# Kernel optimization log

Hardware: AMD Instinct MI355X
Metric: run time of the kernel (lower is better)

Reference implementation:

```python
import jax, jax.numpy as jnp
import numpy as np

WS = (7, 7, 7)
N = WS[0] * WS[1] * WS[2]          # 343 tokens per window
B, D, L, H = 128, 512, 6, 8
DH = D // H                        # 64
DFF = 4 * D
EPS = 1e-5


def _relative_position_index_3d(ws):
    d = np.arange(ws[0]); h = np.arange(ws[1]); w = np.arange(ws[2])
    coords = np.stack(np.meshgrid(d, h, w, indexing='ij'))      # [3, D, H, W]
    cf = coords.reshape(3, -1)                                   # [3, n]
    rel = cf[:, :, None] - cf[:, None, :]                        # [3, n, n]
    rel = rel.transpose(1, 2, 0).copy()                          # [n, n, 3]
    rel[:, :, 0] += ws[0] - 1
    rel[:, :, 1] += ws[1] - 1
    rel[:, :, 2] += ws[2] - 1
    rel[:, :, 0] *= (2 * ws[1] - 1) * (2 * ws[2] - 1)
    rel[:, :, 1] *= 2 * ws[2] - 1
    return rel.sum(-1).astype(np.int32)                          # [n, n]


def setup_inputs() -> dict:
    key = jax.random.key(0)
    ks = jax.random.split(key, 16)
    s = lambda d: 1.0 / np.sqrt(d)
    inp = {
        'x':    jax.random.normal(ks[0], (B, N, D), jnp.float32),
        'Wq':   jax.random.normal(ks[1], (L, D, D), jnp.float32) * s(D),
        'Wk':   jax.random.normal(ks[2], (L, D, D), jnp.float32) * s(D),
        'Wv':   jax.random.normal(ks[3], (L, D, D), jnp.float32) * s(D),
        'Wo':   jax.random.normal(ks[4], (L, D, D), jnp.float32) * s(D),
        'W1ff': jax.random.normal(ks[5], (L, D, DFF), jnp.float32) * s(D),
        'b1ff': jnp.zeros((L, DFF), jnp.float32),
        'W2ff': jax.random.normal(ks[6], (L, DFF, D), jnp.float32) * s(DFF),
        'b2ff': jnp.zeros((L, D), jnp.float32),
        'ln1_g': jnp.ones((L, D), jnp.float32),
        'ln1_b': jnp.zeros((L, D), jnp.float32),
        'ln2_g': jnp.ones((L, D), jnp.float32),
        'ln2_b': jnp.zeros((L, D), jnp.float32),
        'lnf_g': jnp.ones((D,), jnp.float32),
        'lnf_b': jnp.zeros((D,), jnp.float32),
        'rel_table': jax.random.normal(ks[7], ((2 * WS[0] - 1) * (2 * WS[1] - 1) * (2 * WS[2] - 1), H), jnp.float32) * 0.02,
        'cpb_w1': jax.random.normal(ks[8], (H, 512), jnp.float32) * s(H),
        'cpb_b1': jax.random.normal(ks[9], (512,), jnp.float32) * 0.02,
        'cpb_w2': jax.random.normal(ks[10], (512, H), jnp.float32) * s(512),
        'rel_index': jnp.asarray(_relative_position_index_3d(WS)),
    }
    return inp


def _layer_norm(x, g, b):
    mu = jnp.mean(x, -1, keepdims=True)
    xc = x - mu
    var = jnp.mean(xc * xc, -1, keepdims=True)
    return xc * jax.lax.rsqrt(var + EPS) * g + b


def _rel_pos_bias(rel_table, cpb_w1, cpb_b1, cpb_w2, rel_index):
    # cpb_mlp: Linear(H->512) + ReLU + Linear(512->H, no bias)
    t = jax.nn.relu(rel_table @ cpb_w1 + cpb_b1) @ cpb_w2        # [T, H]
    bias = t[rel_index.reshape(-1)].reshape(N, N, H)             # gather -> [n, n, H]
    return jnp.transpose(bias, (2, 0, 1))                        # [H, n, n]


def reference(x, Wq, Wk, Wv, Wo, W1ff, b1ff, W2ff, b2ff,
              ln1_g, ln1_b, ln2_g, ln2_b, lnf_g, lnf_b,
              rel_table, cpb_w1, cpb_b1, cpb_w2, rel_index):
    bias = _rel_pos_bias(rel_table, cpb_w1, cpb_b1, cpb_w2, rel_index)  # [H, n, n] shared across layers
    scale = DH ** -0.5
    for l in range(L):
        # --- attention block (pre-norm) ---
        h = _layer_norm(x, ln1_g[l], ln1_b[l])
        q = (h @ Wq[l]).reshape(B, N, H, DH)
        k = (h @ Wk[l]).reshape(B, N, H, DH)
        v = (h @ Wv[l]).reshape(B, N, H, DH)
        scores = jnp.einsum('bihd,bjhd->bhij', q, k) * scale + bias[None]
        attn = jax.nn.softmax(scores, axis=-1)
        o = jnp.einsum('bhij,bjhd->bihd', attn, v).reshape(B, N, D)
        x = x + o @ Wo[l]
        # --- feed-forward block (pre-norm) ---
        h = _layer_norm(x, ln2_g[l], ln2_b[l])
        x = x + jax.nn.gelu(h @ W1ff[l] + b1ff[l]) @ W2ff[l] + b2ff[l]
    return _layer_norm(x, lnf_g, lnf_b)
```

## Files before the change

### kernel.cpp

```cpp
#include <hip/hip_runtime.h>

typedef __attribute__((ext_vector_type(8))) short short8;
typedef __attribute__((ext_vector_type(4))) float fx4;
typedef __attribute__((ext_vector_type(4))) int ix4;

#define MFMA16(a, b, c) __builtin_amdgcn_mfma_f32_16x16x32_bf16((a), (b), (c), 0, 0, 0)

__device__ __forceinline__ short f2bf(float f) {
  unsigned u = __float_as_uint(f);
  u += 0x7fffu + ((u >> 16) & 1u);
  return (short)(u >> 16);
}
__device__ __forceinline__ float bf2f(short v) {
  return __uint_as_float(((unsigned)(unsigned short)v) << 16);
}
__device__ __forceinline__ void glds16(const short* g, short* l) {
  __builtin_amdgcn_global_load_lds((const __attribute__((address_space(1))) void*)g,
                                   (__attribute__((address_space(3))) void*)l, 16, 0, 0);
}
__device__ __forceinline__ unsigned lds_off(const void* p) {
  return (unsigned)(uintptr_t)(const __attribute__((address_space(3))) void*)p;
}
__device__ __forceinline__ ix4 ds_read128(unsigned addr) {
  ix4 r;
  asm volatile("ds_read_b128 %0, %1" : "=v"(r) : "v"(addr));
  return r;
}
#define LGKM(N)                                             \
  asm volatile("s_waitcnt lgkmcnt(" #N ")" ::: "memory");   \
  __builtin_amdgcn_sched_barrier(0)

__global__ __launch_bounds__(256)
void transpose_cvt(const float* __restrict__ W, short* __restrict__ Wt, int K, int N) {
  __shared__ float tile[64][65];
  const int kb = blockIdx.x * 64, nb = blockIdx.y * 64;
  const int t = threadIdx.x;
  const int tr = t >> 6, tc = t & 63;
#pragma unroll 4
  for (int i = 0; i < 16; i++) {
    int r = i * 4 + tr;
    tile[r][tc] = W[(size_t)(kb + r) * N + nb + tc];
  }
  __syncthreads();
#pragma unroll 4
  for (int i = 0; i < 16; i++) {
    int r = i * 4 + tr;
    Wt[(size_t)(nb + r) * K + kb + tc] = f2bf(tile[tc][r]);
  }
}

__global__ __launch_bounds__(256)
void cpb_kernel(const float* __restrict__ rt, const float* __restrict__ w1,
                const float* __restrict__ b1, const float* __restrict__ w2,
                float* __restrict__ tt) {
  const int id = blockIdx.x * 256 + threadIdx.x;
  if (id >= 2197 * 8) return;
  const int row = id >> 3, hh = id & 7;
  float r[8];
#pragma unroll
  for (int i = 0; i < 8; i++) r[i] = rt[row * 8 + i];
  float acc = 0.0f;
  for (int c = 0; c < 512; c++) {
    float s = b1[c];
#pragma unroll
    for (int i = 0; i < 8; i++) s += r[i] * w1[i * 512 + c];
    s = fmaxf(s, 0.0f);
    acc += s * w2[c * 8 + hh];
  }
  tt[id] = acc;
}

__global__ __launch_bounds__(256)
void build_biasfrag(const float* __restrict__ tt, const int* __restrict__ ridx,
                    short* __restrict__ biasb) {
  const int id = blockIdx.x * 256 + threadIdx.x;
  if (id >= 8 * 22 * 11 * 512) return;
  const int e = id & 7;
  const int lane = (id >> 3) & 63;
  const int rest = id >> 9;
  const int jp = rest % 11;
  const int rest2 = rest / 11;
  const int qt = rest2 % 22;
  const int h = rest2 / 22;
  const int q = qt * 16 + ((lane >> 4) << 2) + (e & 3);
  const int tok = (jp * 2 + (e >> 2)) * 16 + (lane & 15);
  float val = -1e30f;
  if (q < 343 && tok < 343) val = tt[ridx[q * 343 + tok] * 8 + h];
  biasb[id] = f2bf(val);
}

template <bool BF16OUT>
__global__ __launch_bounds__(256)
void ln_kernel(const float* x, const float* __restrict__ g,
               const float* __restrict__ bb, void* out) {
  const int row = blockIdx.x * 4 + (threadIdx.x >> 6);
  const int lane = threadIdx.x & 63;
  const float* xr = x + (size_t)row * 512 + lane * 8;
  fx4 va = *(const fx4*)xr;
  fx4 vb = *(const fx4*)(xr + 4);
  float s = va[0] + va[1] + va[2] + va[3] + vb[0] + vb[1] + vb[2] + vb[3];
#pragma unroll
  for (int d = 1; d < 64; d <<= 1) s += __shfl_xor(s, d);
  const float mu = s * (1.0f / 512.0f);
  float v[8];
#pragma unroll
  for (int i = 0; i < 4; i++) { v[i] = va[i] - mu; v[4 + i] = vb[i] - mu; }
  float s2 = 0.0f;
#pragma unroll
  for (int i = 0; i < 8; i++) s2 += v[i] * v[i];
#pragma unroll
  for (int d = 1; d < 64; d <<= 1) s2 += __shfl_xor(s2, d);
  const float rs = rsqrtf(s2 * (1.0f / 512.0f) + 1e-5f);
  fx4 ga = *(const fx4*)(g + lane * 8);
  fx4 gb = *(const fx4*)(g + lane * 8 + 4);
  fx4 ba = *(const fx4*)(bb + lane * 8);
  fx4 b2 = *(const fx4*)(bb + lane * 8 + 4);
  float o[8];
#pragma unroll
  for (int i = 0; i < 4; i++) {
    o[i] = v[i] * rs * ga[i] + ba[i];
    o[4 + i] = v[4 + i] * rs * gb[i] + b2[i];
  }
  if (BF16OUT) {
    short8 ov;
#pragma unroll
    for (int i = 0; i < 8; i++) ov[i] = f2bf(o[i]);
    *(short8*)((short*)out + (size_t)row * 512 + lane * 8) = ov;
  } else {
    float* op = (float*)out + (size_t)row * 512 + lane * 8;
    fx4 o1, o2;
#pragma unroll
    for (int i = 0; i < 4; i++) { o1[i] = o[i]; o2[i] = o[4 + i]; }
    *(fx4*)op = o1;
    *(fx4*)(op + 4) = o2;
  }
}

template <int EPI>
__global__ __launch_bounds__(256, 3)
void gemm_s(const short* __restrict__ A, const short* __restrict__ Bt,
            int N, int K, int nbn, int scaleN,
            const float* __restrict__ bias, const float* xres, void* out) {
  __shared__ short Al[3][4096];
  __shared__ short Bl[3][4096];
  const int nwg = gridDim.x;
  const int orig = blockIdx.x;
  const int qq = nwg >> 3, rr = nwg & 7, xc = orig & 7, o8 = orig >> 3;
  const int wgid = (xc < rr ? xc * (qq + 1) : rr * (qq + 1) + (xc - rr) * qq) + o8;
  const int m0 = (wgid / nbn) * 128, n0 = (wgid % nbn) * 128;
  const int t = threadIdx.x, lane = t & 63, wv = t >> 6;
  const int lr = lane & 15, lg = lane >> 4;
  const int scol = ((lane & 3) * 8) ^ ((lane & 32) ? 16 : 0);
  const int srow = lane >> 2;
  const short* ag0 = A + (size_t)(m0 + wv * 32 + srow) * K + scol;
  const short* ag1 = A + (size_t)(m0 + wv * 32 + 16 + srow) * K + scol;
  const short* bg0 = Bt + (size_t)(n0 + wv * 32 + srow) * K + scol;
  const short* bg1 = Bt + (size_t)(n0 + wv * 32 + 16 + srow) * K + scol;
  const int cswz = (lg * 8) ^ ((lr & 8) ? 16 : 0);
  const unsigned abase = lds_off(&Al[0][0]);
  const unsigned bbase = lds_off(&Bl[0][0]);
  unsigned aoffB[4], boffB[4];
#pragma unroll
  for (int i = 0; i < 4; i++) {
    aoffB[i] = (((wv >> 1) * 4 + i) * 512 + lr * 32 + cswz) * 2u;
    boffB[i] = (((wv & 1) * 4 + i) * 512 + lr * 32 + cswz) * 2u;
  }
  fx4 acc[4][4] = {};
#define STAGE(KT, BUF)                              \
  do {                                              \
    const int off_ = (KT) * 32;                     \
    short* la_ = &Al[BUF][wv * 1024];               \
    short* lb_ = &Bl[BUF][wv * 1024];               \
    glds16(ag0 + off_, la_);                        \
    glds16(ag1 + off_, la_ + 512);                  \
    glds16(bg0 + off_, lb_);                        \
    glds16(bg1 + off_, lb_ + 512);                  \
  } while (0)
  const int nkt = K >> 5;
  STAGE(0, 0);
  STAGE(1, 1);
  int rb = 0;
  for (int kt = 0; kt < nkt; kt++) {
    if (kt + 1 < nkt)
      asm volatile("s_waitcnt vmcnt(4)" ::: "memory");
    else
      asm volatile("s_waitcnt vmcnt(0)" ::: "memory");
    __builtin_amdgcn_s_barrier();
    if (kt + 2 < nkt) {
      int sb = rb + 2;
      if (sb >= 3) sb -= 3;
      STAGE(kt + 2, sb);
    }
    const unsigned ab = abase + (unsigned)rb * 8192u;
    const unsigned bb_ = bbase + (unsigned)rb * 8192u;
    ix4 a0 = ds_read128(ab + aoffB[0]);
    ix4 b0 = ds_read128(bb_ + boffB[0]);
    ix4 b1 = ds_read128(bb_ + boffB[1]);
    ix4 b2 = ds_read128(bb_ + boffB[2]);
    ix4 b3 = ds_read128(bb_ + boffB[3]);
    ix4 a1 = ds_read128(ab + aoffB[1]);
    ix4 a2 = ds_read128(ab + aoffB[2]);
    ix4 a3 = ds_read128(ab + aoffB[3]);
    const short8 B0 = __builtin_bit_cast(short8, b0);
    const short8 B1 = __builtin_bit_cast(short8, b1);
    const short8 B2 = __builtin_bit_cast(short8, b2);
    const short8 B3 = __builtin_bit_cast(short8, b3);
    LGKM(3);
    {
      const short8 Af = __builtin_bit_cast(short8, a0);
      acc[0][0] = MFMA16(Af, B0, acc[0][0]);
      acc[0][1] = MFMA16(Af, B1, acc[0][1]);
      acc[0][2] = MFMA16(Af, B2, acc[0][2]);
      acc[0][3] = MFMA16(Af, B3, acc[0][3]);
    }
    LGKM(2);
    {
      const short8 Af = __builtin_bit_cast(short8, a1);
      acc[1][0] = MFMA16(Af, B0, acc[1][0]);
      acc[1][1] = MFMA16(Af, B1, acc[1][1]);
      acc[1][2] = MFMA16(Af, B2, acc[1][2]);
      acc[1][3] = MFMA16(Af, B3, acc[1][3]);
    }
    LGKM(1);
    {
      const short8 Af = __builtin_bit_cast(short8, a2);
      acc[2][0] = MFMA16(Af, B0, acc[2][0]);
      acc[2][1] = MFMA16(Af, B1, acc[2][1]);
      acc[2][2] = MFMA16(Af, B2, acc[2][2]);
      acc[2][3] = MFMA16(Af, B3, acc[2][3]);
    }
    LGKM(0);
    {
      const short8 Af = __builtin_bit_cast(short8, a3);
      acc[3][0] = MFMA16(Af, B0, acc[3][0]);
      acc[3][1] = MFMA16(Af, B1, acc[3][1]);
      acc[3][2] = MFMA16(Af, B2, acc[3][2]);
      acc[3][3] = MFMA16(Af, B3, acc[3][3]);
    }
    rb = (rb + 1 < 3) ? rb + 1 : 0;
  }
#undef STAGE
#pragma unroll
  for (int mi = 0; mi < 4; mi++) {
#pragma unroll
    for (int ni = 0; ni < 4; ni++) {
#pragma unroll
      for (int r = 0; r < 4; r++) {
        const int row = m0 + (wv >> 1) * 64 + mi * 16 + lg * 4 + r;
        const int col = n0 + (wv & 1) * 64 + ni * 16 + lr;
        const float vacc = acc[mi][ni][r];
        const size_t idx = (size_t)row * N + col;
        if (EPI == 0) {
          const float sc = (col < scaleN) ? 0.125f : 1.0f;
          ((short*)out)[idx] = f2bf(vacc * sc);
        } else if (EPI == 1) {
          ((float*)out)[idx] = xres[idx] + vacc;
        } else if (EPI == 2) {
          const float v = vacc + bias[col];
          const float tt = v * v;
          const float u2 = v * fmaf(tt, -0.0713548165f, -1.5957691216f);
          const float g = v * __builtin_amdgcn_rcpf(1.0f + __expf(u2));
          ((short*)out)[idx] = f2bf(g);
        } else {
          ((float*)out)[idx] = xres[idx] + vacc + bias[col];
        }
      }
    }
  }
}

__global__ __launch_bounds__(512, 1)
void attn_kernel(const short* __restrict__ qkv, const short* __restrict__ biasb,
                 short* __restrict__ obuf) {
  __shared__ short Kl[352][72];
  __shared__ short Vt[64][360];
  __shared__ short Pl[8][16][96];
  const int b = blockIdx.x >> 3, h = blockIdx.x & 7;
  const int t = threadIdx.x, lane = t & 63, wv = t >> 6;
  const int lr = lane & 15, lg = lane >> 4;
  const size_t base = (size_t)b * 343 * 1536 + h * 64;
  const short* qg = qkv + base;
  const short* kg = qkv + base + 512;
  const short* vg = qkv + base + 1024;
  for (int c = t; c < 352 * 8; c += 512) {
    const int tok = c >> 3, d8 = (c & 7) * 8;
    const int ts = tok < 343 ? tok : 342;
    short8 kvv = *(const short8*)(kg + (size_t)ts * 1536 + d8);
    short8 vvv = *(const short8*)(vg + (size_t)ts * 1536 + d8);
    *(short8*)&Kl[tok][d8] = kvv;
#pragma unroll
    for (int j = 0; j < 8; j++) Vt[d8 + j][tok] = vvv[j];
  }
  __syncthreads();
  for (int qt = wv; qt < 22; qt += 8) {
    const int q0 = qt * 16;
    const int qr = q0 + lr;
    const int qs = qr < 343 ? qr : 342;
    short8 qf0 = *(const short8*)(qg + (size_t)qs * 1536 + lg * 8);
    short8 qf1 = *(const short8*)(qg + (size_t)qs * 1536 + 32 + lg * 8);
    fx4 s[22];
#pragma unroll
    for (int j = 0; j < 22; j++) {
      short8 kf0 = *(const short8*)&Kl[j * 16 + lr][lg * 8];
      short8 kf1 = *(const short8*)&Kl[j * 16 + lr][32 + lg * 8];
      fx4 z = {0.0f, 0.0f, 0.0f, 0.0f};
      z = MFMA16(qf0, kf0, z);
      z = MFMA16(qf1, kf1, z);
      s[j] = z;
    }
    const short* bp = biasb + (size_t)((h * 22 + qt) * 11) * 512 + lane * 8;
#pragma unroll
    for (int jp = 0; jp < 11; jp++) {
      short8 bb = *(const short8*)(bp + jp * 512);
#pragma unroll
      for (int r = 0; r < 4; r++) {
        s[2 * jp][r] += bf2f(bb[r]);
        s[2 * jp + 1][r] += bf2f(bb[4 + r]);
      }
    }
    float mx[4] = {-1e30f, -1e30f, -1e30f, -1e30f};
#pragma unroll
    for (int j = 0; j < 22; j++)
#pragma unroll
      for (int r = 0; r < 4; r++) mx[r] = fmaxf(mx[r], s[j][r]);
#pragma unroll
    for (int r = 0; r < 4; r++) {
      float m = mx[r];
      m = fmaxf(m, __shfl_xor(m, 1));
      m = fmaxf(m, __shfl_xor(m, 2));
      m = fmaxf(m, __shfl_xor(m, 4));
      m = fmaxf(m, __shfl_xor(m, 8));
      mx[r] = m;
    }
    float sm[4] = {0.0f, 0.0f, 0.0f, 0.0f};
#pragma unroll
    for (int j = 0; j < 22; j++)
#pragma unroll
      for (int r = 0; r < 4; r++) {
        const float p = __expf(s[j][r] - mx[r]);
        s[j][r] = p;
        sm[r] += p;
      }
#pragma unroll
    for (int r = 0; r < 4; r++) {
      float ss = sm[r];
      ss += __shfl_xor(ss, 1);
      ss += __shfl_xor(ss, 2);
      ss += __shfl_xor(ss, 4);
      ss += __shfl_xor(ss, 8);
      sm[r] = 1.0f / ss;
    }
    fx4 oacc[4] = {};
#pragma unroll
    for (int c = 0; c < 4; c++) {
      const int nj = (c < 3) ? 6 : 4;
#pragma unroll
      for (int j = 0; j < 6; j++) {
        if (j < nj) {
#pragma unroll
          for (int r = 0; r < 4; r++)
            Pl[wv][lg * 4 + r][j * 16 + lr] = f2bf(s[c * 6 + j][r] * sm[r]);
        }
      }
      const int nk = (c < 3) ? 3 : 2;
#pragma unroll
      for (int ks = 0; ks < 3; ks++) {
        if (ks < nk) {
          short8 pb = *(const short8*)&Pl[wv][lr][ks * 32 + lg * 8];
#pragma unroll
          for (int mi = 0; mi < 4; mi++) {
            short8 vva = *(const short8*)&Vt[mi * 16 + lr][c * 96 + ks * 32 + lg * 8];
            oacc[mi] = MFMA16(vva, pb, oacc[mi]);
          }
        }
      }
    }
    if (qr < 343) {
#pragma unroll
      for (int mi = 0; mi < 4; mi++)
#pragma unroll
        for (int r = 0; r < 4; r++) {
          const int dh = mi * 16 + lg * 4 + r;
          obuf[(size_t)(b * 343 + qr) * 512 + h * 64 + dh] = f2bf(oacc[mi][r]);
        }
    }
  }
}

extern "C" void kernel_launch(void* const* d_in, const int* in_sizes, int n_in,
                              void* d_out, int out_size, void* d_ws, size_t ws_size,
                              hipStream_t stream) {
  const float* x_in = (const float*)d_in[0];
  const float* Wq = (const float*)d_in[1];
  const float* Wk = (const float*)d_in[2];
  const float* Wv = (const float*)d_in[3];
  const float* Wo = (const float*)d_in[4];
  const float* W1 = (const float*)d_in[5];
  const float* b1 = (const float*)d_in[6];
  const float* W2 = (const float*)d_in[7];
  const float* b2 = (const float*)d_in[8];
  const float* ln1g = (const float*)d_in[9];
  const float* ln1b = (const float*)d_in[10];
  const float* ln2g = (const float*)d_in[11];
  const float* ln2b = (const float*)d_in[12];
  const float* lnfg = (const float*)d_in[13];
  const float* lnfb = (const float*)d_in[14];
  const float* rtab = (const float*)d_in[15];
  const float* cw1 = (const float*)d_in[16];
  const float* cb1 = (const float*)d_in[17];
  const float* cw2 = (const float*)d_in[18];
  const int* ridx = (const int*)d_in[19];
  float* xout = (float*)d_out;

  char* p = (char*)d_ws;
  short* wt = (short*)p;      p += 37748736;
  short* hbuf = (short*)p;    p += 44957696;
  char* big = p;              p += 179830784;
  short* biasb = (short*)p;   p += 1982464;
  float* tt = (float*)p;      p += 70304;
  short* qkvbuf = (short*)big;
  short* obuf = (short*)(big + 134873088);
  short* mid = (short*)big;

  cpb_kernel<<<(2197 * 8 + 255) / 256, 256, 0, stream>>>(rtab, cw1, cb1, cw2, tt);
  build_biasfrag<<<(8 * 22 * 11 * 512 + 255) / 256, 256, 0, stream>>>(tt, ridx, biasb);

  for (int l = 0; l < 6; l++) {
    const size_t wl = (size_t)l * 3145728;
    transpose_cvt<<<dim3(8, 8), 256, 0, stream>>>(Wq + (size_t)l * 262144, wt + wl, 512, 512);
    transpose_cvt<<<dim3(8, 8), 256, 0, stream>>>(Wk + (size_t)l * 262144, wt + wl + 262144, 512, 512);
    transpose_cvt<<<dim3(8, 8), 256, 0, stream>>>(Wv + (size_t)l * 262144, wt + wl + 524288, 512, 512);
    transpose_cvt<<<dim3(8, 8), 256, 0, stream>>>(Wo + (size_t)l * 262144, wt + wl + 786432, 512, 512);
    transpose_cvt<<<dim3(8, 32), 256, 0, stream>>>(W1 + (size_t)l * 1048576, wt + wl + 1048576, 512, 2048);
    transpose_cvt<<<dim3(32, 8), 256, 0, stream>>>(W2 + (size_t)l * 1048576, wt + wl + 2097152, 2048, 512);
  }

  for (int l = 0; l < 6; l++) {
    const size_t wl = (size_t)l * 3145728;
    const float* xsrc = (l == 0) ? x_in : xout;
    ln_kernel<true><<<10976, 256, 0, stream>>>(xsrc, ln1g + l * 512, ln1b + l * 512, hbuf);
    gemm_s<0><<<343 * 12, 256, 0, stream>>>(hbuf, wt + wl, 1536, 512, 12, 512, nullptr, nullptr, qkvbuf);
    attn_kernel<<<1024, 512, 0, stream>>>(qkvbuf, biasb, obuf);
    gemm_s<1><<<343 * 4, 256, 0, stream>>>(obuf, wt + wl + 786432, 512, 512, 4, 0, nullptr, xsrc, xout);
    ln_kernel<true><<<10976, 256, 0, stream>>>(xout, ln2g + l * 512, ln2b + l * 512, hbuf);
    gemm_s<2><<<343 * 16, 256, 0, stream>>>(hbuf, wt + wl + 1048576, 2048, 512, 16, 0, b1 + l * 2048, nullptr, mid);
    gemm_s<3><<<343 * 4, 256, 0, stream>>>(mid, wt + wl + 2097152, 512, 2048, 4, 0, b2 + l * 512, xout, xout);
  }
  ln_kernel<false><<<10976, 256, 0, stream>>>(xout, lnfg, lnfb, xout);
}
```

Measured before the change: 4.077 ms.

## Fuse residual add and layer norm into full-row output projection GEMMs

Adds a gemm_ln kernel in which each workgroup computes a 128x512 full-width output tile, so the residual add, bias and the following LayerNorm (ln2, next layer's ln1, or the final norm) can be applied in the epilogue through a cross-wave LDS reduction. This removes the separate ln_kernel launches and their extra read and write of the fp32 activations. The cost is a grid of only 343 workgroups of 512 threads with large per-thread accumulator state, which lowers parallelism and occupancy compared with the previous 1372-block GEMMs. Variance is computed as E[x^2]-mu^2, which is less numerically robust than a two-pass computation.

```diff
diff --git a/kernel.cpp b/kernel.cpp
--- a/kernel.cpp
+++ b/kernel.cpp
@@ -269,6 +269,199 @@
   }
 }
 
+template <int MODE>
+__global__ __launch_bounds__(512, 2)
+void gemm_ln(const short* __restrict__ A, const short* __restrict__ Bt, int K,
+             const float* __restrict__ bias, const float* xres,
+             const float* __restrict__ lng, const float* __restrict__ lnb,
+             float* xout, short* hbuf) {
+  __shared__ short lds3[3][20480];
+  const int nwg = gridDim.x;
+  const int orig = blockIdx.x;
+  const int qq = nwg >> 3, rr2 = nwg & 7, xcd = orig & 7, o8 = orig >> 3;
+  const int wgid = (xcd < rr2 ? xcd * (qq + 1) : rr2 * (qq + 1) + (xcd - rr2) * qq) + o8;
+  const int m0 = wgid * 128;
+  const int t = threadIdx.x, lane = t & 63, wv = t >> 6;
+  const int wave_m = wv >> 2, wave_n = wv & 3;
+  const int lr = lane & 15, lg = lane >> 4;
+  const int scol = ((lane & 3) * 8) ^ ((lane & 32) ? 16 : 0);
+  const int srow = lane >> 2;
+  const short* gsrc[5];
+#pragma unroll
+  for (int j = 0; j < 5; j++) {
+    const int c = wv * 5 + j;
+    gsrc[j] = (c < 8) ? A + (size_t)(m0 + c * 16 + srow) * K + scol
+                      : Bt + (size_t)((c - 8) * 16 + srow) * K + scol;
+  }
+  const int cswz = (lg * 8) ^ ((lr & 8) ? 16 : 0);
+  const unsigned base0 = lds_off(&lds3[0][0]);
+  unsigned aoff[4], boff[8];
+#pragma unroll
+  for (int i = 0; i < 4; i++)
+    aoff[i] = (unsigned)((wave_m * 4 + i) * 512 + lr * 32 + cswz) * 2u;
+#pragma unroll
+  for (int i = 0; i < 8; i++)
+    boff[i] = (unsigned)(4096 + (wave_n * 8 + i) * 512 + lr * 32 + cswz) * 2u;
+  fx4 acc[4][8];
+#pragma unroll
+  for (int mi = 0; mi < 4; mi++)
+#pragma unroll
+    for (int ni = 0; ni < 8; ni++) acc[mi][ni] = fx4{0.f, 0.f, 0.f, 0.f};
+#define STAGE(KT, BUF)                                    \
+  do {                                                    \
+    const size_t koff = (size_t)(KT) * 32;                \
+    short* ld = &lds3[BUF][wv * 2560];                    \
+    _Pragma("unroll") for (int j_ = 0; j_ < 5; j_++)      \
+        glds16(gsrc[j_] + koff, ld + j_ * 512);           \
+  } while (0)
+  const int nkt = K >> 5;
+  STAGE(0, 0);
+  STAGE(1, 1);
+  int rb = 0;
+  for (int kt = 0; kt < nkt; kt++) {
+    if (kt + 1 < nkt)
+      asm volatile("s_waitcnt vmcnt(5)" ::: "memory");
+    else
+      asm volatile("s_waitcnt vmcnt(0)" ::: "memory");
+    __builtin_amdgcn_s_barrier();
+    if (kt + 2 < nkt) {
+      int sb = rb + 2;
+      if (sb >= 3) sb -= 3;
+      STAGE(kt + 2, sb);
+    }
+    const unsigned bufb = base0 + (unsigned)rb * 40960u;
+    ix4 a0 = ds_read128(bufb + aoff[0]);
+    ix4 b0 = ds_read128(bufb + boff[0]);
+    ix4 b1 = ds_read128(bufb + boff[1]);
+    ix4 b2 = ds_read128(bufb + boff[2]);
+    ix4 b3 = ds_read128(bufb + boff[3]);
+    ix4 b4 = ds_read128(bufb + boff[4]);
+    ix4 b5 = ds_read128(bufb + boff[5]);
+    ix4 b6 = ds_read128(bufb + boff[6]);
+    ix4 b7 = ds_read128(bufb + boff[7]);
+    ix4 a1 = ds_read128(bufb + aoff[1]);
+    ix4 a2 = ds_read128(bufb + aoff[2]);
+    ix4 a3 = ds_read128(bufb + aoff[3]);
+    const short8 B0 = __builtin_bit_cast(short8, b0);
+    const short8 B1 = __builtin_bit_cast(short8, b1);
+    const short8 B2 = __builtin_bit_cast(short8, b2);
+    const short8 B3 = __builtin_bit_cast(short8, b3);
+    const short8 B4 = __builtin_bit_cast(short8, b4);
+    const short8 B5 = __builtin_bit_cast(short8, b5);
+    const short8 B6 = __builtin_bit_cast(short8, b6);
+    const short8 B7 = __builtin_bit_cast(short8, b7);
+#define ROW(mi, av)                                                  \
+  {                                                                  \
+    const short8 Af = __builtin_bit_cast(short8, av);                \
+    acc[mi][0] = MFMA16(Af, B0, acc[mi][0]);                         \
+    acc[mi][1] = MFMA16(Af, B1, acc[mi][1]);                         \
+    acc[mi][2] = MFMA16(Af, B2, acc[mi][2]);                         \
+    acc[mi][3] = MFMA16(Af, B3, acc[mi][3]);                         \
+    acc[mi][4] = MFMA16(Af, B4, acc[mi][4]);                         \
+    acc[mi][5] = MFMA16(Af, B5, acc[mi][5]);                         \
+    acc[mi][6] = MFMA16(Af, B6, acc[mi][6]);                         \
+    acc[mi][7] = MFMA16(Af, B7, acc[mi][7]);                         \
+  }
+    LGKM(3);
+    ROW(0, a0);
+    LGKM(2);
+    ROW(1, a1);
+    LGKM(1);
+    ROW(2, a2);
+    LGKM(0);
+    ROW(3, a3);
+#undef ROW
+    rb = (rb + 1 < 3) ? rb + 1 : 0;
+  }
+#undef STAGE
+  __syncthreads();
+  float gc[8], bc[8], bcol[8];
+#pragma unroll
+  for (int ni = 0; ni < 8; ni++) {
+    const int col = wave_n * 128 + ni * 16 + lr;
+    gc[ni] = lng[col];
+    bc[ni] = lnb[col];
+    bcol[ni] = (MODE != 0) ? bias[col] : 0.0f;
+  }
+  float s_[4][4], q_[4][4];
+#pragma unroll
+  for (int mi = 0; mi < 4; mi++)
+#pragma unroll
+    for (int rr = 0; rr < 4; rr++) { s_[mi][rr] = 0.f; q_[mi][rr] = 0.f; }
+#pragma unroll
+  for (int mi = 0; mi < 4; mi++) {
+#pragma unroll
+    for (int ni = 0; ni < 8; ni++) {
+#pragma unroll
+      for (int rr = 0; rr < 4; rr++) {
+        const int row = m0 + wave_m * 64 + mi * 16 + lg * 4 + rr;
+        const int col = wave_n * 128 + ni * 16 + lr;
+        const size_t idx = (size_t)row * 512 + col;
+        const float v = acc[mi][ni][rr] + bcol[ni] + xres[idx];
+        acc[mi][ni][rr] = v;
+        s_[mi][rr] += v;
+        q_[mi][rr] += v * v;
+      }
+    }
+  }
+#pragma unroll
+  for (int mi = 0; mi < 4; mi++)
+#pragma unroll
+    for (int rr = 0; rr < 4; rr++) {
+      float s = s_[mi][rr], q = q_[mi][rr];
+      s += __shfl_xor(s, 1); q += __shfl_xor(q, 1);
+      s += __shfl_xor(s, 2); q += __shfl_xor(q, 2);
+      s += __shfl_xor(s, 4); q += __shfl_xor(q, 4);
+      s += __shfl_xor(s, 8); q += __shfl_xor(q, 8);
+      s_[mi][rr] = s; q_[mi][rr] = q;
+    }
+  float* red = (float*)&lds3[0][0];
+  if (lr == 0) {
+#pragma unroll
+    for (int mi = 0; mi < 4; mi++)
+#pragma unroll
+      for (int rr = 0; rr < 4; rr++) {
+        const int rl = wave_m * 64 + mi * 16 + lg * 4 + rr;
+        red[(wave_n * 128 + rl) * 2] = s_[mi][rr];
+        red[(wave_n * 128 + rl) * 2 + 1] = q_[mi][rr];
+      }
+  }
+  __syncthreads();
+  float mu_[4][4], rs_[4][4];
+#pragma unroll
+  for (int mi = 0; mi < 4; mi++)
+#pragma unroll
+    for (int rr = 0; rr < 4; rr++) {
+      const int rl = wave_m * 64 + mi * 16 + lg * 4 + rr;
+      const float sum = red[rl * 2] + red[(128 + rl) * 2] + red[(256 + rl) * 2] + red[(384 + rl) * 2];
+      const float sq = red[rl * 2 + 1] + red[(128 + rl) * 2 + 1] + red[(256 + rl) * 2 + 1] + red[(384 + rl) * 2 + 1];
+      const float mu = sum * (1.0f / 512.0f);
+      const float var = sq * (1.0f / 512.0f) - mu * mu;
+      mu_[mi][rr] = mu;
+      rs_[mi][rr] = rsqrtf(var + 1e-5f);
+    }
+#pragma unroll
+  for (int mi = 0; mi < 4; mi++) {
+#pragma unroll
+    for (int ni = 0; ni < 8; ni++) {
+#pragma unroll
+      for (int rr = 0; rr < 4; rr++) {
+        const int row = m0 + wave_m * 64 + mi * 16 + lg * 4 + rr;
+        const int col = wave_n * 128 + ni * 16 + lr;
+        const size_t idx = (size_t)row * 512 + col;
+        const float v = acc[mi][ni][rr];
+        const float ln = (v - mu_[mi][rr]) * rs_[mi][rr] * gc[ni] + bc[ni];
+        if (MODE < 2) {
+          xout[idx] = v;
+          hbuf[idx] = f2bf(ln);
+        } else {
+          xout[idx] = ln;
+        }
+      }
+    }
+  }
+}
+
 __global__ __launch_bounds__(512, 1)
 void attn_kernel(const short* __restrict__ qkv, const short* __restrict__ biasb,
                  short* __restrict__ obuf) {
@@ -435,16 +628,22 @@
     transpose_cvt<<<dim3(32, 8), 256, 0, stream>>>(W2 + (size_t)l * 1048576, wt + wl + 2097152, 2048, 512);
   }
 
+  ln_kernel<true><<<10976, 256, 0, stream>>>(x_in, ln1g, ln1b, hbuf);
+
   for (int l = 0; l < 6; l++) {
     const size_t wl = (size_t)l * 3145728;
     const float* xsrc = (l == 0) ? x_in : xout;
-    ln_kernel<true><<<10976, 256, 0, stream>>>(xsrc, ln1g + l * 512, ln1b + l * 512, hbuf);
     gemm_s<0><<<343 * 12, 256, 0, stream>>>(hbuf, wt + wl, 1536, 512, 12, 512, nullptr, nullptr, qkvbuf);
     attn_kernel<<<1024, 512, 0, stream>>>(qkvbuf, biasb, obuf);
-    gemm_s<1><<<343 * 4, 256, 0, stream>>>(obuf, wt + wl + 786432, 512, 512, 4, 0, nullptr, xsrc, xout);
-    ln_kernel<true><<<10976, 256, 0, stream>>>(xout, ln2g + l * 512, ln2b + l * 512, hbuf);
+    gemm_ln<0><<<343, 512, 0, stream>>>(obuf, wt + wl + 786432, 512, nullptr, xsrc,
+                                        ln2g + l * 512, ln2b + l * 512, xout, hbuf);
     gemm_s<2><<<343 * 16, 256, 0, stream>>>(hbuf, wt + wl + 1048576, 2048, 512, 16, 0, b1 + l * 2048, nullptr, mid);
-    gemm_s<3><<<343 * 4, 256, 0, stream>>>(mid, wt + wl + 2097152, 512, 2048, 4, 0, b2 + l * 512, xout, xout);
-  }
-  ln_kernel<false><<<10976, 256, 0, stream>>>(xout, lnfg, lnfb, xout);
-}
+    if (l < 5) {
+      gemm_ln<1><<<343, 512, 0, stream>>>(mid, wt + wl + 2097152, 2048, b2 + l * 512, xout,
+                                          ln1g + (l + 1) * 512, ln1b + (l + 1) * 512, xout, hbuf);
+    } else {
+      gemm_ln<2><<<343, 512, 0, stream>>>(mid, wt + wl + 2097152, 2048, b2 + l * 512, xout,
+                                          lnfg, lnfb, xout, nullptr);
+    }
+  }
+}
```

New measurement: 4.183 ms. +2.6%, slower.
